# Kernel tuning notes

Measured on AMD Instinct MI355X. Metric: run time of the kernel, lower is better.

The kernel has to match this reference:

```python
import jax, jax.numpy as jnp
import numpy as np

B, H, S, D = 2, 16, 2048, 128
BS = 128  # block_size
NB = S // BS  # num_blocks
SPARSITY_PROB = 0.5


def setup_inputs() -> dict:
    key = jax.random.key(0)
    kq, kk, kv, km = jax.random.split(key, 4)
    query = jax.random.normal(kq, (B, H, S, D), dtype=jnp.float32)
    k_ = jax.random.normal(kk, (B, H, S, D), dtype=jnp.float32)
    v_ = jax.random.normal(kv, (B, H, S, D), dtype=jnp.float32)
    # block pattern: rand < sparsity_prob, diagonal forced True (causal=False)
    block_mask = jax.random.uniform(km, (NB, NB)) < SPARSITY_PROB
    block_mask = block_mask | jnp.eye(NB, dtype=bool)
    return {"query": query, "key": k_, "value": v_,
            "block_mask": block_mask, "block_size": BS}


def reference(query, key, value, block_mask, block_size):
    b, h, s, d = query.shape
    nb = s // block_size
    scale = 1.0 / jnp.sqrt(jnp.float32(d))
    # reshape into blocks: (b, h, nb, bs, d)
    qb = query.reshape(b, h, nb, block_size, d)
    kb = key.reshape(b, h, nb, block_size, d)
    vb = value.reshape(b, h, nb, block_size, d)
    # per-(i,j)-block scores: (b, h, i, j, q, k)
    scores = jnp.einsum('bhiqd,bhjkd->bhijqk', qb, kb) * scale
    # IMPORTANT: softmax is taken independently within each block (axis=-1),
    # matching the original's per-block (non-merged) softmax.
    attn = jax.nn.softmax(scores, axis=-1)
    # zero out inactive blocks, then sum contributions over j
    attn = attn * block_mask[None, None, :, :, None, None].astype(attn.dtype)
    out = jnp.einsum('bhijqk,bhjkd->bhiqd', attn, vb)
    return out.reshape(b, h, s, d)
```

## Files before the change

kernel.cpp:

```cpp
#include <hip/hip_runtime.h>
#include <stdint.h>

#define BDIM 256

typedef __attribute__((ext_vector_type(8))) short short8;
typedef __attribute__((ext_vector_type(4))) float f32x4;

__device__ __forceinline__ unsigned f2bf(float f) {
    union { float f; unsigned u; } a; a.f = f;
    unsigned r = a.u + 0x7fffu + ((a.u >> 16) & 1u);
    return (r >> 16) & 0xffffu;
}
__device__ __forceinline__ float f4e(float4 v, int e) {
    return e == 0 ? v.x : e == 1 ? v.y : e == 2 ? v.z : v.w;
}
__device__ __forceinline__ unsigned u4e(uint4 v, int e) {
    return e == 0 ? v.x : e == 1 ? v.y : e == 2 ? v.z : v.w;
}
__device__ __forceinline__ uint2 shfl_u2(uint2 v, int src) {
    uint2 r;
    r.x = (unsigned)__shfl((int)v.x, src);
    r.y = (unsigned)__shfl((int)v.y, src);
    return r;
}
__device__ __forceinline__ bool detect_bf16(const void* p) {
    unsigned w = ((const unsigned*)p)[threadIdx.x & 63];
    unsigned lo = w & 0xffffu, ex = (lo >> 7) & 0xffu;
    bool pl = (lo == 0u) || (ex >= 0x68u && ex <= 0x86u);
    return __popcll(__ballot(pl)) >= 40;
}

__global__ __launch_bounds__(BDIM)
void convert_kernel(const void* __restrict__ src, uint2* __restrict__ dst, int n4)
{
    bool isBf = detect_bf16(src);
    int stride = gridDim.x * BDIM;
    for (int t = blockIdx.x * BDIM + threadIdx.x; t < n4; t += stride) {
        uint2 o;
        if (isBf) {
            o = ((const uint2*)src)[t];
        } else {
            float4 v = ((const float4*)src)[t];
            o.x = f2bf(v.x) | (f2bf(v.y) << 16);
            o.y = f2bf(v.z) | (f2bf(v.w) << 16);
        }
        dst[t] = o;
    }
}

template<bool QF32, bool KVF32>
__device__ __forceinline__ void attn_body(const void* Qv, const void* Kv,
                                          const void* Vv,
                                          const unsigned char* Mb, bool maskByte,
                                          void* Ov, char* ldsK, char* ldsV,
                                          int bh, int i)
{
    constexpr int S = 2048, D = 128;
    const int tid  = threadIdx.x;
    const int lane = tid & 63;
    const int wave = tid >> 6;
    const int quad = lane >> 4;
    const int l16  = lane & 15;

    const int qb0 = wave * 32;
    const size_t qrowbase = ((size_t)bh * S + (size_t)i * 128) * D;

    short8 qf[2][4];
#pragma unroll
    for (int nt = 0; nt < 2; ++nt) {
        int qrow = qb0 + nt * 16 + l16;
#pragma unroll
        for (int ks = 0; ks < 4; ++ks) {
            int dof = ks * 32 + quad * 8;
            if constexpr (QF32) {
                const float* qp = (const float*)Qv + qrowbase + (size_t)qrow * D + dof;
                float4 f0 = *(const float4*)qp;
                float4 f1 = *(const float4*)(qp + 4);
                short8 v;
                v[0] = (short)f2bf(f0.x); v[1] = (short)f2bf(f0.y);
                v[2] = (short)f2bf(f0.z); v[3] = (short)f2bf(f0.w);
                v[4] = (short)f2bf(f1.x); v[5] = (short)f2bf(f1.y);
                v[6] = (short)f2bf(f1.z); v[7] = (short)f2bf(f1.w);
                qf[nt][ks] = v;
            } else {
                qf[nt][ks] = *(const short8*)((const unsigned short*)Qv
                              + qrowbase + (size_t)qrow * D + dof);
            }
        }
    }

    f32x4 accO[2][8];
#pragma unroll
    for (int a = 0; a < 2; ++a)
#pragma unroll
        for (int b = 0; b < 8; ++b)
            accO[a][b] = (f32x4){0.f, 0.f, 0.f, 0.f};

    const float C2 = 0.08838834764831845f * 1.44269504088896f;
    const int srcA = l16 + ((quad & 1) << 5);
    const int srcB = srcA + 16;
    const bool hiMs = (quad >> 1) != 0;

    for (int j = 0; j < 16; ++j) {
        bool active = maskByte ? (Mb[i * 16 + j] != 0)
                               : (((const int*)Mb)[i * 16 + j] != 0);
        if (!active) continue;

        __syncthreads();
        const size_t kb = ((size_t)bh * S + (size_t)j * 128) * D;

        if constexpr (KVF32) {
#pragma unroll
            for (int it = 0; it < 16; ++it) {
                int f = it * BDIM + tid;
                int r = f >> 5, c4 = f & 31;
                float4 v = ((const float4*)((const float*)Kv + kb))[f];
                uint2 pk;
                pk.x = f2bf(v.x) | (f2bf(v.y) << 16);
                pk.y = f2bf(v.z) | (f2bf(v.w) << 16);
                int ch = c4 >> 1;
                *(uint2*)(ldsK + r * 256 + ((ch ^ (r & 7)) << 4)
                          + ((c4 & 1) << 3)) = pk;
            }
        } else {
#pragma unroll
            for (int it = 0; it < 8; ++it) {
                int id = it * BDIM + tid;
                int r = id >> 4, ch = id & 15;
                uint4 v = ((const uint4*)((const unsigned short*)Kv + kb))[id];
                *(uint4*)(ldsK + r * 256 + ((ch ^ (r & 7)) << 4)) = v;
            }
        }

#pragma unroll
        for (int it = 0; it < 2; ++it) {
            int id = it * BDIM + tid, pp = id & 31, dc = id >> 5;
            if constexpr (KVF32) {
                const float* vb = (const float*)Vv + kb + (size_t)(4 * pp) * D + dc * 8;
                float4 ra[4], rb[4];
#pragma unroll
                for (int r = 0; r < 4; ++r) {
                    ra[r] = *(const float4*)(vb + (size_t)r * D);
                    rb[r] = *(const float4*)(vb + (size_t)r * D + 4);
                }
#pragma unroll
                for (int e = 0; e < 8; ++e) {
                    float v0 = (e < 4) ? f4e(ra[0], e) : f4e(rb[0], e - 4);
                    float v1 = (e < 4) ? f4e(ra[1], e) : f4e(rb[1], e - 4);
                    float v2 = (e < 4) ? f4e(ra[2], e) : f4e(rb[2], e - 4);
                    float v3 = (e < 4) ? f4e(ra[3], e) : f4e(rb[3], e - 4);
                    uint2 pk;
                    pk.x = f2bf(v0) | (f2bf(v1) << 16);
                    pk.y = f2bf(v2) | (f2bf(v3) << 16);
                    int d = dc * 8 + e;
                    *(uint2*)(ldsV + d * 256 + (((pp >> 1) ^ (d & 7)) << 4)
                              + ((pp & 1) << 3)) = pk;
                }
            } else {
                const unsigned short* vb = (const unsigned short*)Vv + kb
                                           + (size_t)(4 * pp) * D + dc * 8;
                uint4 r0 = *(const uint4*)(vb);
                uint4 r1 = *(const uint4*)(vb + D);
                uint4 r2 = *(const uint4*)(vb + 2 * D);
                uint4 r3 = *(const uint4*)(vb + 3 * D);
#pragma unroll
                for (int e = 0; e < 8; ++e) {
                    unsigned h0 = u4e(r0, e >> 1), h1 = u4e(r1, e >> 1);
                    unsigned h2 = u4e(r2, e >> 1), h3 = u4e(r3, e >> 1);
                    if (e & 1) { h0 >>= 16; h1 >>= 16; h2 >>= 16; h3 >>= 16; }
                    uint2 pk;
                    pk.x = (h0 & 0xffffu) | (h1 << 16);
                    pk.y = (h2 & 0xffffu) | (h3 << 16);
                    int d = dc * 8 + e;
                    *(uint2*)(ldsV + d * 256 + (((pp >> 1) ^ (d & 7)) << 4)
                              + ((pp & 1) << 3)) = pk;
                }
            }
        }
        __syncthreads();

        f32x4 accS[2][8];
#pragma unroll
        for (int nt = 0; nt < 2; ++nt)
#pragma unroll
            for (int mt = 0; mt < 8; ++mt)
                accS[nt][mt] = (f32x4){0.f, 0.f, 0.f, 0.f};

#pragma unroll
        for (int mt = 0; mt < 8; ++mt) {
            int r = mt * 16 + l16;
            short8 kf[4];
#pragma unroll
            for (int ks = 0; ks < 4; ++ks) {
                int c = ks * 4 + quad;
                kf[ks] = *(const short8*)(ldsK + r * 256 + ((c ^ (r & 7)) << 4));
            }
#pragma unroll
            for (int nt = 0; nt < 2; ++nt)
#pragma unroll
                for (int ks = 0; ks < 4; ++ks)
                    accS[nt][mt] = __builtin_amdgcn_mfma_f32_16x16x32_bf16(
                        kf[ks], qf[nt][ks], accS[nt][mt], 0, 0, 0);
        }

        uint2 p2[2][8];
#pragma unroll
        for (int nt = 0; nt < 2; ++nt) {
            float mx = -3.0e38f;
#pragma unroll
            for (int mt = 0; mt < 8; ++mt)
#pragma unroll
                for (int rr = 0; rr < 4; ++rr)
                    mx = fmaxf(mx, accS[nt][mt][rr]);
            mx = fmaxf(mx, __shfl_xor(mx, 16));
            mx = fmaxf(mx, __shfl_xor(mx, 32));
            float mc = mx * C2;
            float sum = 0.f;
#pragma unroll
            for (int mt = 0; mt < 8; ++mt)
#pragma unroll
                for (int rr = 0; rr < 4; ++rr) {
                    float p = exp2f(accS[nt][mt][rr] * C2 - mc);
                    accS[nt][mt][rr] = p;
                    sum += p;
                }
            sum += __shfl_xor(sum, 16);
            sum += __shfl_xor(sum, 32);
            float rinv = 1.0f / sum;
#pragma unroll
            for (int mt = 0; mt < 8; ++mt) {
                p2[nt][mt].x = f2bf(accS[nt][mt][0] * rinv)
                             | (f2bf(accS[nt][mt][1] * rinv) << 16);
                p2[nt][mt].y = f2bf(accS[nt][mt][2] * rinv)
                             | (f2bf(accS[nt][mt][3] * rinv) << 16);
            }
        }

#pragma unroll
        for (int ks = 0; ks < 4; ++ks) {
            short8 pf[2];
#pragma unroll
            for (int nt = 0; nt < 2; ++nt) {
                uint2 a0 = shfl_u2(p2[nt][2 * ks + 0], srcA);
                uint2 a1 = shfl_u2(p2[nt][2 * ks + 1], srcA);
                uint2 b0 = shfl_u2(p2[nt][2 * ks + 0], srcB);
                uint2 b1 = shfl_u2(p2[nt][2 * ks + 1], srcB);
                uint2 lo, hi;
                lo.x = hiMs ? a1.x : a0.x;  lo.y = hiMs ? a1.y : a0.y;
                hi.x = hiMs ? b1.x : b0.x;  hi.y = hiMs ? b1.y : b0.y;
                union { uint4 u; short8 s; } w;
                w.u.x = lo.x; w.u.y = lo.y; w.u.z = hi.x; w.u.w = hi.y;
                pf[nt] = w.s;
            }
#pragma unroll
            for (int dt = 0; dt < 8; ++dt) {
                int d = dt * 16 + l16;
                int c = ks * 4 + quad;
                short8 vf = *(const short8*)(ldsV + d * 256 + ((c ^ (d & 7)) << 4));
                accO[0][dt] = __builtin_amdgcn_mfma_f32_16x16x32_bf16(
                    pf[0], vf, accO[0][dt], 0, 0, 0);
                accO[1][dt] = __builtin_amdgcn_mfma_f32_16x16x32_bf16(
                    pf[1], vf, accO[1][dt], 0, 0, 0);
            }
        }
    }

#pragma unroll
    for (int mt = 0; mt < 2; ++mt)
#pragma unroll
        for (int rr = 0; rr < 4; ++rr) {
            int qrow = qb0 + mt * 16 + quad * 4 + rr;
#pragma unroll
            for (int nt = 0; nt < 8; ++nt) {
                size_t idx = qrowbase + (size_t)qrow * D + nt * 16 + l16;
                if constexpr (QF32)
                    ((float*)Ov)[idx] = accO[mt][nt][rr];
                else
                    ((unsigned short*)Ov)[idx] = (unsigned short)f2bf(accO[mt][nt][rr]);
            }
        }
}

__device__ __forceinline__ void swizzle_bhi(int blk, int& bh, int& i) {
    bh = ((blk >> 7) << 3) | (blk & 7);
    i  = (blk >> 3) & 15;
}

__global__ __launch_bounds__(BDIM, 2)
void attn_ws(const void* __restrict__ Q, const unsigned short* __restrict__ Kb,
             const unsigned short* __restrict__ Vb,
             const unsigned char* __restrict__ Mb, void* __restrict__ O)
{
    __shared__ uint4 ldsK4[2048];
    __shared__ uint4 ldsV4[2048];
    int bh, i; swizzle_bhi(blockIdx.x, bh, i);
    bool qBf = detect_bf16(Q);
    unsigned mu = ((const unsigned*)Mb)[threadIdx.x & 63];
    bool maskByte = (__ballot((mu & 0xFFFFFF00u) != 0u) != 0ull);
    if (qBf)
        attn_body<false, false>(Q, Kb, Vb, Mb, maskByte, O,
                                (char*)ldsK4, (char*)ldsV4, bh, i);
    else
        attn_body<true, false>(Q, Kb, Vb, Mb, maskByte, O,
                               (char*)ldsK4, (char*)ldsV4, bh, i);
}

__global__ __launch_bounds__(BDIM, 2)
void attn_direct(const void* __restrict__ Q, const void* __restrict__ K,
                 const void* __restrict__ V,
                 const unsigned char* __restrict__ Mb, void* __restrict__ O)
{
    __shared__ uint4 ldsK4[2048];
    __shared__ uint4 ldsV4[2048];
    int bh, i; swizzle_bhi(blockIdx.x, bh, i);
    bool qBf = detect_bf16(Q);
    unsigned mu = ((const unsigned*)Mb)[threadIdx.x & 63];
    bool maskByte = (__ballot((mu & 0xFFFFFF00u) != 0u) != 0ull);
    if (qBf)
        attn_body<false, false>(Q, K, V, Mb, maskByte, O,
                                (char*)ldsK4, (char*)ldsV4, bh, i);
    else
        attn_body<true, true>(Q, K, V, Mb, maskByte, O,
                              (char*)ldsK4, (char*)ldsV4, bh, i);
}

extern "C" void kernel_launch(void* const* d_in, const int* in_sizes, int n_in,
                              void* d_out, int out_size, void* d_ws, size_t ws_size,
                              hipStream_t stream) {
    const int NK = 2 * 16 * 2048 * 128;
    const size_t need = (size_t)NK * 2 * 2;
    if (ws_size >= need) {
        unsigned short* Kb = (unsigned short*)d_ws;
        unsigned short* Vb = Kb + NK;
        convert_kernel<<<2048, BDIM, 0, stream>>>(d_in[1], (uint2*)Kb, NK / 4);
        convert_kernel<<<2048, BDIM, 0, stream>>>(d_in[2], (uint2*)Vb, NK / 4);
        attn_ws<<<512, BDIM, 0, stream>>>(d_in[0], Kb, Vb,
                                          (const unsigned char*)d_in[3], d_out);
    } else {
        attn_direct<<<512, BDIM, 0, stream>>>(d_in[0], d_in[1], d_in[2],
                                              (const unsigned char*)d_in[3], d_out);
    }
}
```

Baseline: 233.4 us.

## Use 8 waves per attention block and fuse K/V conversion launches

The attention kernel now runs 512 threads per block, with each wave handling 16 query rows instead of 32. This halves per-wave accumulator registers and spreads K/V staging across more threads. The two bf16 conversion launches are merged into one kernel covering both K and V, which removes a launch. The risk is that K/V LDS tiles are now amortised over fewer query rows per wave, and larger blocks may sync more expensively.

```diff
diff --git a/kernel.cpp b/kernel.cpp
--- a/kernel.cpp
+++ b/kernel.cpp
@@ -1,7 +1,8 @@
 #include <hip/hip_runtime.h>
 #include <stdint.h>
 
-#define BDIM 256
+#define BDIM_C 256
+#define BDIM_A 512
 
 typedef __attribute__((ext_vector_type(8))) short short8;
 typedef __attribute__((ext_vector_type(4))) float f32x4;
@@ -30,21 +31,25 @@
     return __popcll(__ballot(pl)) >= 40;
 }
 
-__global__ __launch_bounds__(BDIM)
-void convert_kernel(const void* __restrict__ src, uint2* __restrict__ dst, int n4)
+__global__ __launch_bounds__(BDIM_C)
+void convert2_kernel(const void* __restrict__ srcK, const void* __restrict__ srcV,
+                     uint2* __restrict__ dstK, uint2* __restrict__ dstV, int n4)
 {
-    bool isBf = detect_bf16(src);
-    int stride = gridDim.x * BDIM;
-    for (int t = blockIdx.x * BDIM + threadIdx.x; t < n4; t += stride) {
+    bool isBf = detect_bf16(srcK);
+    int stride = gridDim.x * BDIM_C;
+    for (int t = blockIdx.x * BDIM_C + threadIdx.x; t < 2 * n4; t += stride) {
+        const void* s = (t < n4) ? srcK : srcV;
+        uint2* d = (t < n4) ? dstK : dstV;
+        int idx = (t < n4) ? t : t - n4;
         uint2 o;
         if (isBf) {
-            o = ((const uint2*)src)[t];
+            o = ((const uint2*)s)[idx];
         } else {
-            float4 v = ((const float4*)src)[t];
+            float4 v = ((const float4*)s)[idx];
             o.x = f2bf(v.x) | (f2bf(v.y) << 16);
             o.y = f2bf(v.z) | (f2bf(v.w) << 16);
         }
-        dst[t] = o;
+        d[idx] = o;
     }
 }
 
@@ -62,13 +67,12 @@
     const int quad = lane >> 4;
     const int l16  = lane & 15;
 
-    const int qb0 = wave * 32;
+    const int qb0 = wave * 16;
     const size_t qrowbase = ((size_t)bh * S + (size_t)i * 128) * D;
 
-    short8 qf[2][4];
-#pragma unroll
-    for (int nt = 0; nt < 2; ++nt) {
-        int qrow = qb0 + nt * 16 + l16;
+    short8 qf[4];
+    {
+        int qrow = qb0 + l16;
 #pragma unroll
         for (int ks = 0; ks < 4; ++ks) {
             int dof = ks * 32 + quad * 8;
@@ -81,20 +85,18 @@
                 v[2] = (short)f2bf(f0.z); v[3] = (short)f2bf(f0.w);
                 v[4] = (short)f2bf(f1.x); v[5] = (short)f2bf(f1.y);
                 v[6] = (short)f2bf(f1.z); v[7] = (short)f2bf(f1.w);
-                qf[nt][ks] = v;
+                qf[ks] = v;
             } else {
-                qf[nt][ks] = *(const short8*)((const unsigned short*)Qv
-                              + qrowbase + (size_t)qrow * D + dof);
-            }
-        }
-    }
-
-    f32x4 accO[2][8];
-#pragma unroll
-    for (int a = 0; a < 2; ++a)
-#pragma unroll
-        for (int b = 0; b < 8; ++b)
-            accO[a][b] = (f32x4){0.f, 0.f, 0.f, 0.f};
+                qf[ks] = *(const short8*)((const unsigned short*)Qv
+                          + qrowbase + (size_t)qrow * D + dof);
+            }
+        }
+    }
+
+    f32x4 accO[8];
+#pragma unroll
+    for (int b = 0; b < 8; ++b)
+        accO[b] = (f32x4){0.f, 0.f, 0.f, 0.f};
 
     const float C2 = 0.08838834764831845f * 1.44269504088896f;
     const int srcA = l16 + ((quad & 1) << 5);
@@ -111,8 +113,8 @@
 
         if constexpr (KVF32) {
 #pragma unroll
-            for (int it = 0; it < 16; ++it) {
-                int f = it * BDIM + tid;
+            for (int it = 0; it < 8; ++it) {
+                int f = it * BDIM_A + tid;
                 int r = f >> 5, c4 = f & 31;
                 float4 v = ((const float4*)((const float*)Kv + kb))[f];
                 uint2 pk;
@@ -124,17 +126,16 @@
             }
         } else {
 #pragma unroll
-            for (int it = 0; it < 8; ++it) {
-                int id = it * BDIM + tid;
+            for (int it = 0; it < 4; ++it) {
+                int id = it * BDIM_A + tid;
                 int r = id >> 4, ch = id & 15;
                 uint4 v = ((const uint4*)((const unsigned short*)Kv + kb))[id];
                 *(uint4*)(ldsK + r * 256 + ((ch ^ (r & 7)) << 4)) = v;
             }
         }
 
-#pragma unroll
-        for (int it = 0; it < 2; ++it) {
-            int id = it * BDIM + tid, pp = id & 31, dc = id >> 5;
+        {
+            int pp = tid & 31, dc = tid >> 5;
             if constexpr (KVF32) {
                 const float* vb = (const float*)Vv + kb + (size_t)(4 * pp) * D + dc * 8;
                 float4 ra[4], rb[4];
@@ -179,12 +180,10 @@
         }
         __syncthreads();
 
-        f32x4 accS[2][8];
-#pragma unroll
-        for (int nt = 0; nt < 2; ++nt)
-#pragma unroll
-            for (int mt = 0; mt < 8; ++mt)
-                accS[nt][mt] = (f32x4){0.f, 0.f, 0.f, 0.f};
+        f32x4 accS[8];
+#pragma unroll
+        for (int mt = 0; mt < 8; ++mt)
+            accS[mt] = (f32x4){0.f, 0.f, 0.f, 0.f};
 
 #pragma unroll
         for (int mt = 0; mt < 8; ++mt) {
@@ -196,22 +195,19 @@
                 kf[ks] = *(const short8*)(ldsK + r * 256 + ((c ^ (r & 7)) << 4));
             }
 #pragma unroll
-            for (int nt = 0; nt < 2; ++nt)
-#pragma unroll
-                for (int ks = 0; ks < 4; ++ks)
-                    accS[nt][mt] = __builtin_amdgcn_mfma_f32_16x16x32_bf16(
-                        kf[ks], qf[nt][ks], accS[nt][mt], 0, 0, 0);
-        }
-
-        uint2 p2[2][8];
-#pragma unroll
-        for (int nt = 0; nt < 2; ++nt) {
+            for (int ks = 0; ks < 4; ++ks)
+                accS[mt] = __builtin_amdgcn_mfma_f32_16x16x32_bf16(
+                    kf[ks], qf[ks], accS[mt], 0, 0, 0);
+        }
+
+        uint2 p2[8];
+        {
             float mx = -3.0e38f;
 #pragma unroll
             for (int mt = 0; mt < 8; ++mt)
 #pragma unroll
                 for (int rr = 0; rr < 4; ++rr)
-                    mx = fmaxf(mx, accS[nt][mt][rr]);
+                    mx = fmaxf(mx, accS[mt][rr]);
             mx = fmaxf(mx, __shfl_xor(mx, 16));
             mx = fmaxf(mx, __shfl_xor(mx, 32));
             float mc = mx * C2;
@@ -220,8 +216,8 @@
             for (int mt = 0; mt < 8; ++mt)
 #pragma unroll
                 for (int rr = 0; rr < 4; ++rr) {
-                    float p = exp2f(accS[nt][mt][rr] * C2 - mc);
-                    accS[nt][mt][rr] = p;
+                    float p = exp2f(accS[mt][rr] * C2 - mc);
+                    accS[mt][rr] = p;
                     sum += p;
                 }
             sum += __shfl_xor(sum, 16);
@@ -229,56 +225,49 @@
             float rinv = 1.0f / sum;
 #pragma unroll
             for (int mt = 0; mt < 8; ++mt) {
-                p2[nt][mt].x = f2bf(accS[nt][mt][0] * rinv)
-                             | (f2bf(accS[nt][mt][1] * rinv) << 16);
-                p2[nt][mt].y = f2bf(accS[nt][mt][2] * rinv)
-                             | (f2bf(accS[nt][mt][3] * rinv) << 16);
+                p2[mt].x = f2bf(accS[mt][0] * rinv) | (f2bf(accS[mt][1] * rinv) << 16);
+                p2[mt].y = f2bf(accS[mt][2] * rinv) | (f2bf(accS[mt][3] * rinv) << 16);
             }
         }
 
 #pragma unroll
         for (int ks = 0; ks < 4; ++ks) {
-            short8 pf[2];
-#pragma unroll
-            for (int nt = 0; nt < 2; ++nt) {
-                uint2 a0 = shfl_u2(p2[nt][2 * ks + 0], srcA);
-                uint2 a1 = shfl_u2(p2[nt][2 * ks + 1], srcA);
-                uint2 b0 = shfl_u2(p2[nt][2 * ks + 0], srcB);
-                uint2 b1 = shfl_u2(p2[nt][2 * ks + 1], srcB);
+            short8 pf;
+            {
+                uint2 a0 = shfl_u2(p2[2 * ks + 0], srcA);
+                uint2 a1 = shfl_u2(p2[2 * ks + 1], srcA);
+                uint2 b0 = shfl_u2(p2[2 * ks + 0], srcB);
+                uint2 b1 = shfl_u2(p2[2 * ks + 1], srcB);
                 uint2 lo, hi;
                 lo.x = hiMs ? a1.x : a0.x;  lo.y = hiMs ? a1.y : a0.y;
                 hi.x = hiMs ? b1.x : b0.x;  hi.y = hiMs ? b1.y : b0.y;
                 union { uint4 u; short8 s; } w;
                 w.u.x = lo.x; w.u.y = lo.y; w.u.z = hi.x; w.u.w = hi.y;
-                pf[nt] = w.s;
+                pf = w.s;
             }
 #pragma unroll
             for (int dt = 0; dt < 8; ++dt) {
                 int d = dt * 16 + l16;
                 int c = ks * 4 + quad;
                 short8 vf = *(const short8*)(ldsV + d * 256 + ((c ^ (d & 7)) << 4));
-                accO[0][dt] = __builtin_amdgcn_mfma_f32_16x16x32_bf16(
-                    pf[0], vf, accO[0][dt], 0, 0, 0);
-                accO[1][dt] = __builtin_amdgcn_mfma_f32_16x16x32_bf16(
-                    pf[1], vf, accO[1][dt], 0, 0, 0);
-            }
-        }
-    }
-
-#pragma unroll
-    for (int mt = 0; mt < 2; ++mt)
-#pragma unroll
-        for (int rr = 0; rr < 4; ++rr) {
-            int qrow = qb0 + mt * 16 + quad * 4 + rr;
-#pragma unroll
-            for (int nt = 0; nt < 8; ++nt) {
-                size_t idx = qrowbase + (size_t)qrow * D + nt * 16 + l16;
-                if constexpr (QF32)
-                    ((float*)Ov)[idx] = accO[mt][nt][rr];
-                else
-                    ((unsigned short*)Ov)[idx] = (unsigned short)f2bf(accO[mt][nt][rr]);
-            }
-        }
+                accO[dt] = __builtin_amdgcn_mfma_f32_16x16x32_bf16(
+                    pf, vf, accO[dt], 0, 0, 0);
+            }
+        }
+    }
+
+#pragma unroll
+    for (int rr = 0; rr < 4; ++rr) {
+        int qrow = qb0 + quad * 4 + rr;
+#pragma unroll
+        for (int dt = 0; dt < 8; ++dt) {
+            size_t idx = qrowbase + (size_t)qrow * D + dt * 16 + l16;
+            if constexpr (QF32)
+                ((float*)Ov)[idx] = accO[dt][rr];
+            else
+                ((unsigned short*)Ov)[idx] = (unsigned short)f2bf(accO[dt][rr]);
+        }
+    }
 }
 
 __device__ __forceinline__ void swizzle_bhi(int blk, int& bh, int& i) {
@@ -286,7 +275,7 @@
     i  = (blk >> 3) & 15;
 }
 
-__global__ __launch_bounds__(BDIM, 2)
+__global__ __launch_bounds__(BDIM_A, 4)
 void attn_ws(const void* __restrict__ Q, const unsigned short* __restrict__ Kb,
              const unsigned short* __restrict__ Vb,
              const unsigned char* __restrict__ Mb, void* __restrict__ O)
@@ -305,7 +294,7 @@
                                (char*)ldsK4, (char*)ldsV4, bh, i);
 }
 
-__global__ __launch_bounds__(BDIM, 2)
+__global__ __launch_bounds__(BDIM_A, 4)
 void attn_direct(const void* __restrict__ Q, const void* __restrict__ K,
                  const void* __restrict__ V,
                  const unsigned char* __restrict__ Mb, void* __restrict__ O)
@@ -332,12 +321,12 @@
     if (ws_size >= need) {
         unsigned short* Kb = (unsigned short*)d_ws;
         unsigned short* Vb = Kb + NK;
-        convert_kernel<<<2048, BDIM, 0, stream>>>(d_in[1], (uint2*)Kb, NK / 4);
-        convert_kernel<<<2048, BDIM, 0, stream>>>(d_in[2], (uint2*)Vb, NK / 4);
-        attn_ws<<<512, BDIM, 0, stream>>>(d_in[0], Kb, Vb,
-                                          (const unsigned char*)d_in[3], d_out);
+        convert2_kernel<<<4096, BDIM_C, 0, stream>>>(d_in[1], d_in[2],
+                                                     (uint2*)Kb, (uint2*)Vb, NK / 4);
+        attn_ws<<<512, BDIM_A, 0, stream>>>(d_in[0], Kb, Vb,
+                                            (const unsigned char*)d_in[3], d_out);
     } else {
-        attn_direct<<<512, BDIM, 0, stream>>>(d_in[0], d_in[1], d_in[2],
-                                              (const unsigned char*)d_in[3], d_out);
-    }
-}
+        attn_direct<<<512, BDIM_A, 0, stream>>>(d_in[0], d_in[1], d_in[2],
+                                                (const unsigned char*)d_in[3], d_out);
+    }
+}
```

Result: no change. 235.2 us (+0.8%).
